# Performance work log

Measured on AMD Instinct MI355X. Metric: run time of the kernel, lower is better.

The kernel has to match this reference:

```python
import jax, jax.numpy as jnp
import numpy as np

H_MODEL = 1024
N_HEADS = 16
N_KV_HEADS = 4
HEAD_DIM = 64
SLIDING_WINDOW = 512
B, S = 2, 2048
NEG_INF = -1e9


def rotate_half(x):
    half = x.shape[-1] // 2
    return jnp.concatenate([-x[..., half:], x[..., :half]], axis=-1)


def setup_inputs() -> dict:
    key = jax.random.key(0)
    ks = jax.random.split(key, 8)
    hidden_states = jax.random.normal(ks[0], (B, S, H_MODEL), dtype=jnp.float32)
    # RoPE tables (HF style): cos/sin of shape [1, S, head_dim]
    inv_freq = 1.0 / (10000.0 ** (jnp.arange(0, HEAD_DIM, 2, dtype=jnp.float32) / HEAD_DIM))
    pos = jnp.arange(S, dtype=jnp.float32)
    freqs = jnp.einsum('s,d->sd', pos, inv_freq)            # [S, D/2]
    emb = jnp.concatenate([freqs, freqs], axis=-1)          # [S, D]
    cos = jnp.cos(emb)[None]                                # [1, S, D]
    sin = jnp.sin(emb)[None]
    # additive causal + sliding-window mask [1,1,S,S]
    i = jnp.arange(S)[:, None]
    j = jnp.arange(S)[None, :]
    allowed = (j <= i) & (i - j < SLIDING_WINDOW)
    attention_mask = jnp.where(allowed, 0.0, NEG_INF).astype(jnp.float32)[None, None]
    # projection weights (torch Linear stores [out, in]; y = x @ W.T)
    std = 0.02
    Wq = jax.random.normal(ks[1], (N_HEADS * HEAD_DIM, H_MODEL), dtype=jnp.float32) * std
    Wk = jax.random.normal(ks[2], (N_KV_HEADS * HEAD_DIM, H_MODEL), dtype=jnp.float32) * std
    Wv = jax.random.normal(ks[3], (N_KV_HEADS * HEAD_DIM, H_MODEL), dtype=jnp.float32) * std
    Wo = jax.random.normal(ks[4], (H_MODEL, N_HEADS * HEAD_DIM), dtype=jnp.float32) * std
    return {"hidden_states": hidden_states, "cos": cos, "sin": sin,
            "attention_mask": attention_mask, "Wq": Wq, "Wk": Wk, "Wv": Wv, "Wo": Wo}


def reference(hidden_states, cos, sin, attention_mask, Wq, Wk, Wv, Wo):
    b, s, _ = hidden_states.shape
    G = N_HEADS // N_KV_HEADS
    scaling = HEAD_DIM ** -0.5
    # QKV projections -> [B, H, S, D]
    q = jnp.einsum('bsh,oh->bso', hidden_states, Wq).reshape(b, s, N_HEADS, HEAD_DIM).transpose(0, 2, 1, 3)
    k = jnp.einsum('bsh,oh->bso', hidden_states, Wk).reshape(b, s, N_KV_HEADS, HEAD_DIM).transpose(0, 2, 1, 3)
    v = jnp.einsum('bsh,oh->bso', hidden_states, Wv).reshape(b, s, N_KV_HEADS, HEAD_DIM).transpose(0, 2, 1, 3)
    # RoPE (cos/sin broadcast over head dim via unsqueeze(1))
    c = cos[:, None, :, :]
    sn = sin[:, None, :, :]
    q = q * c + rotate_half(q) * sn
    k = k * c + rotate_half(k) * sn
    # GQA eager attention: group query heads over kv heads
    qg = q.reshape(b, N_KV_HEADS, G, s, HEAD_DIM)
    scores = jnp.einsum('bkgqd,bkpd->bkgqp', qg, k) * scaling  # [B,Hkv,G,S,S]
    scores = scores + attention_mask[:, :, None, :, :]
    probs = jax.nn.softmax(scores.astype(jnp.float32), axis=-1).astype(q.dtype)
    out = jnp.einsum('bkgqp,bkpd->bkgqd', probs, v)            # [B,Hkv,G,S,D]
    out = out.reshape(b, N_HEADS, s, HEAD_DIM).transpose(0, 2, 1, 3).reshape(b, s, N_HEADS * HEAD_DIM)
    return jnp.einsum('bso,ho->bsh', out, Wo)
```

## Files before the change

### kernel.cpp

```cpp
#include <hip/hip_runtime.h>
#include <hip/hip_bf16.h>

#define S_LEN 2048
#define NH 16
#define NKV 4
#define HD 64
#define WIN 512
#define BATCH 2

typedef __bf16 bf16_8 __attribute__((ext_vector_type(8)));
typedef float f32x4 __attribute__((ext_vector_type(4)));

__device__ inline bf16_8 cvt8(f32x4 a, f32x4 b) {
    bf16_8 r;
    r[0] = (__bf16)a[0]; r[1] = (__bf16)a[1]; r[2] = (__bf16)a[2]; r[3] = (__bf16)a[3];
    r[4] = (__bf16)b[0]; r[5] = (__bf16)b[1]; r[6] = (__bf16)b[2]; r[7] = (__bf16)b[3];
    return r;
}

typedef __attribute__((address_space(1))) const unsigned int guint;
typedef __attribute__((address_space(3))) unsigned int luint;
__device__ __forceinline__ void gload16(const void* g, void* l) {
    __builtin_amdgcn_global_load_lds((guint*)g, (luint*)l, 16, 0, 0);
}

__global__ __launch_bounds__(256) void cvt_pack(
    const float* __restrict__ hs, const float* __restrict__ Wq,
    const float* __restrict__ Wk, const float* __restrict__ Wv,
    const float* __restrict__ Wo,
    __bf16* __restrict__ hsb, __bf16* __restrict__ Wqp,
    __bf16* __restrict__ Wkp, __bf16* __restrict__ Wvp,
    __bf16* __restrict__ Wop)
{
    int i = blockIdx.x * 256 + threadIdx.x;
    if (i < 524288) {
        const size_t j = (size_t)i * 8;
        const f32x4 a = *(const f32x4*)(hs + j);
        const f32x4 b = *(const f32x4*)(hs + j + 4);
        *(bf16_8*)(hsb + j) = cvt8(a, b);
        return;
    }
    i -= 524288;
    const float* S; __bf16* P;
    if (i < 131072)      { S = Wq; P = Wqp; }
    else if (i < 163840) { S = Wk; P = Wkp; i -= 131072; }
    else if (i < 196608) { S = Wv; P = Wvp; i -= 163840; }
    else                 { S = Wo; P = Wop; i -= 196608; }
    const int n = i >> 7;
    const int k = (i & 127) << 3;
    const f32x4 a = *(const f32x4*)(S + (size_t)n * 1024 + k);
    const f32x4 b = *(const f32x4*)(S + (size_t)n * 1024 + k + 4);
    const size_t dst = ((size_t)((n >> 4) * 32 + (k >> 5)) << 9)
                     + ((size_t)((n & 15) | (((k >> 3) & 3) << 4)) << 3);
    *(bf16_8*)(P + dst) = cvt8(a, b);
}

__device__ __forceinline__ void gemm64x128(
    const __bf16* __restrict__ Ap, const __bf16* __restrict__ Bq,
    int row0, __bf16* __restrict__ As, int tid, f32x4 acc[2][4])
{
    const int wave = tid >> 6;
    const int lane = tid & 63;
    const int wm   = wave & 1;
    const int fm   = lane & 15;
    const int fj   = (lane >> 4) << 3;
    const f32x4 fzero = {0.f, 0.f, 0.f, 0.f};
#pragma unroll
    for (int i = 0; i < 2; ++i)
#pragma unroll
        for (int nt = 0; nt < 4; ++nt) acc[i][nt] = fzero;

    const int srow = (wave << 4) + (lane >> 3);
    const int xr   = (((lane & 7) << 3)) ^ ((srow & 7) << 3);
    const __bf16* gA = Ap + (size_t)(row0 + srow) * 1024 + xr;
    __bf16* dstB0 = As + wave * 1024;

    const int r0  = wm * 32 + fm;
    const int xk0 = fj ^ ((fm & 7) << 3);
    const int xk1 = xk0 ^ 32;

    gload16(gA, dstB0);
    gload16(gA + 8192, dstB0 + 512);
    bf16_8 b0[4], b1[4];
#pragma unroll
    for (int nt = 0; nt < 4; ++nt) {
        b0[nt] = *(const bf16_8*)(Bq + nt * 16384);
        b1[nt] = *(const bf16_8*)(Bq + nt * 16384 + 512);
    }
    __syncthreads();

#pragma unroll 2
    for (int it = 0; it < 16; ++it) {
        const int cur = it & 1;
        const bool pf = it < 15;
        bf16_8 nb0[4], nb1[4];
        if (pf) {
            __bf16* dst = As + (cur ^ 1) * 4096 + wave * 1024;
            gload16(gA + (it + 1) * 64, dst);
            gload16(gA + (it + 1) * 64 + 8192, dst + 512);
#pragma unroll
            for (int nt = 0; nt < 4; ++nt) {
                nb0[nt] = *(const bf16_8*)(Bq + nt * 16384 + (it + 1) * 1024);
                nb1[nt] = *(const bf16_8*)(Bq + nt * 16384 + (it + 1) * 1024 + 512);
            }
        }

        const __bf16* Ab = As + cur * 4096;
        bf16_8 af0[2];
        af0[0] = *(const bf16_8*)&Ab[r0 * 64 + xk0];
        af0[1] = *(const bf16_8*)&Ab[(r0 + 16) * 64 + xk0];
#pragma unroll
        for (int i = 0; i < 2; ++i)
#pragma unroll
            for (int nt = 0; nt < 4; ++nt)
                acc[i][nt] = __builtin_amdgcn_mfma_f32_16x16x32_bf16(af0[i], b0[nt], acc[i][nt], 0, 0, 0);

        bf16_8 af1[2];
        af1[0] = *(const bf16_8*)&Ab[r0 * 64 + xk1];
        af1[1] = *(const bf16_8*)&Ab[(r0 + 16) * 64 + xk1];
#pragma unroll
        for (int i = 0; i < 2; ++i)
#pragma unroll
            for (int nt = 0; nt < 4; ++nt)
                acc[i][nt] = __builtin_amdgcn_mfma_f32_16x16x32_bf16(af1[i], b1[nt], acc[i][nt], 0, 0, 0);

        if (pf) {
#pragma unroll
            for (int nt = 0; nt < 4; ++nt) { b0[nt] = nb0[nt]; b1[nt] = nb1[nt]; }
        }
        __syncthreads();
    }
}

__global__ __launch_bounds__(256) void gemm_qkv(
    const __bf16* __restrict__ A,
    const __bf16* __restrict__ Wqp,
    const __bf16* __restrict__ Wkp,
    const __bf16* __restrict__ Wvp,
    __bf16* __restrict__ Qb,
    __bf16* __restrict__ Kf,
    __bf16* __restrict__ Vf,
    const float* __restrict__ cosb,
    const float* __restrict__ sinb)
{
    __shared__ __align__(16) __bf16 smem[9216];

    const int tid  = threadIdx.x;
    const int wave = tid >> 6;
    const int lane = tid & 63;
    const int wm   = wave & 1;
    const int wn   = wave >> 1;
    const int fm   = lane & 15;

    const int row0 = blockIdx.x * 64;
    const int by   = blockIdx.y;

    const __bf16* Bp; int colb; int mode;
    if (by < 8)       { Bp = Wqp; colb = by * 128;        mode = 0; }
    else if (by < 10) { Bp = Wkp; colb = (by - 8) * 128;  mode = 1; }
    else              { Bp = Wvp; colb = (by - 10) * 128; mode = 2; }
    const int col0 = colb;

    const __bf16* Bq = Bp + (size_t)((colb + wn * 64) >> 4) * 16384 + (lane << 3);
    f32x4 acc[2][4];
    gemm64x128(A, Bq, row0, smem, tid, acc);

    const int drow = (lane >> 4) << 2;
    const int cq   = col0 + wn * 64;
    const int bb   = row0 >> 11;
    const int sk0  = row0 & (S_LEN - 1);

    if (mode == 0) {
#pragma unroll
        for (int i = 0; i < 2; ++i) {
#pragma unroll
            for (int r = 0; r < 4; ++r) {
                const int row = row0 + wm * 32 + i * 16 + drow + r;
                const int s   = row & (S_LEN - 1);
#pragma unroll
                for (int nt = 0; nt < 2; ++nt) {
                    const int d = nt * 16 + fm;
                    const float c1 = cosb[s * HD + d];
                    const float s1 = sinb[s * HD + d];
                    const float c2 = cosb[s * HD + d + 32];
                    const float s2 = sinb[s * HD + d + 32];
                    const float x1 = acc[i][nt][r];
                    const float x2 = acc[i][nt + 2][r];
                    Qb[(size_t)row * 1024 + cq + d]      = (__bf16)(x1 * c1 - x2 * s1);
                    Qb[(size_t)row * 1024 + cq + d + 32] = (__bf16)(x2 * c2 + x1 * s2);
                }
            }
        }
    } else if (mode == 1) {
        __bf16* T = smem;
#pragma unroll
        for (int i = 0; i < 2; ++i) {
#pragma unroll
            for (int r = 0; r < 4; ++r) {
                const int kl = wm * 32 + i * 16 + drow + r;
                const int s  = sk0 + kl;
#pragma unroll
                for (int nt = 0; nt < 2; ++nt) {
                    const int d = nt * 16 + fm;
                    const float c1 = cosb[s * HD + d];
                    const float s1 = sinb[s * HD + d];
                    const float c2 = cosb[s * HD + d + 32];
                    const float s2 = sinb[s * HD + d + 32];
                    const float x1 = acc[i][nt][r];
                    const float x2 = acc[i][nt + 2][r];
                    T[kl * 136 + wn * 64 + d]      = (__bf16)(x1 * c1 - x2 * s1);
                    T[kl * 136 + wn * 64 + d + 32] = (__bf16)(x2 * c2 + x1 * s2);
                }
            }
        }
        __syncthreads();
#pragma unroll
        for (int c = 0; c < 4; ++c) {
            const int tile = c * 4 + wave;
            const int hh  = tile >> 3;
            const int kt4 = (tile >> 1) & 3;
            const int dd  = tile & 1;
            const int key = kt4 * 16 + fm;
            const int dl  = dd * 32 + ((lane >> 4) << 3);
            const bf16_8 v = *(const bf16_8*)&T[key * 136 + hh * 64 + dl];
            const int khg = (col0 + hh * 64) >> 6;
            const int ktg = (sk0 >> 4) + kt4;
            *(bf16_8*)&Kf[(size_t)(bb * NKV + khg) * 131072 + (size_t)(ktg * 2 + dd) * 512 + lane * 8] = v;
        }
    } else {
        __bf16* T2 = smem;
#pragma unroll
        for (int i = 0; i < 2; ++i)
#pragma unroll
            for (int r = 0; r < 4; ++r)
#pragma unroll
                for (int nt = 0; nt < 4; ++nt)
                    T2[(wn * 64 + nt * 16 + fm) * 72 + wm * 32 + i * 16 + drow + r] =
                        (__bf16)acc[i][nt][r];
        __syncthreads();
#pragma unroll
        for (int c = 0; c < 4; ++c) {
            const int tile = c * 4 + wave;
            const int hh  = tile >> 3;
            const int dd4 = (tile >> 1) & 3;
            const int ks  = tile & 1;
            const int dl  = dd4 * 16 + fm;
            const int key = ks * 32 + ((lane >> 4) << 3);
            const bf16_8 v = *(const bf16_8*)&T2[(hh * 64 + dl) * 72 + key];
            const int khg = (col0 + hh * 64) >> 6;
            const int kvg = (sk0 >> 5) + ks;
            *(bf16_8*)&Vf[(size_t)(bb * NKV + khg) * 131072 + (size_t)(dd4 * 64 + kvg) * 512 + lane * 8] = v;
        }
    }
}

__global__ __launch_bounds__(256) void gemm_o(
    const __bf16* __restrict__ A,
    const __bf16* __restrict__ Bp,
    float* __restrict__ C)
{
    __shared__ __align__(16) __bf16 smem[9216];

    const int tid  = threadIdx.x;
    const int wave = tid >> 6;
    const int lane = tid & 63;
    const int wm   = wave & 1;
    const int wn   = wave >> 1;

    const int row0 = blockIdx.x * 64;
    const int colb = blockIdx.y * 128;

    const __bf16* Bq = Bp + (size_t)((colb + wn * 64) >> 4) * 16384 + (lane << 3);
    f32x4 acc[2][4];
    gemm64x128(A, Bq, row0, smem, tid, acc);

    const int fm = lane & 15;
    const int drow = (lane >> 4) << 2;
#pragma unroll
    for (int i = 0; i < 2; ++i)
#pragma unroll
        for (int r = 0; r < 4; ++r) {
            const int row = row0 + wm * 32 + i * 16 + drow + r;
#pragma unroll
            for (int nt = 0; nt < 4; ++nt)
                C[(size_t)row * 1024 + colb + wn * 64 + nt * 16 + fm] = acc[i][nt][r];
        }
}

__global__ __launch_bounds__(256) void attn_pk(const __bf16* __restrict__ Q,
                                               const __bf16* __restrict__ Kf,
                                               const __bf16* __restrict__ Vf,
                                               __bf16* __restrict__ O)
{
    __shared__ __align__(16) __bf16 Ps[4][16][72];

    const int tid  = threadIdx.x;
    const int wave = tid >> 6;
    const int lane = tid & 63;

    const int bid0 = blockIdx.x;
    const int bid  = (bid0 & 7) * 128 + (bid0 >> 3);

    const int qt = bid & (S_LEN / 64 - 1);
    const int h  = (bid >> 5) & (NH - 1);
    const int b  = bid >> 9;
    const int kh = h >> 2;

    const int q0 = qt * 64;
    const int qw = q0 + wave * 16;

    const int fm = lane & 15;
    const int fj = (lane >> 4) << 3;

    const size_t qrow = (size_t)(b * S_LEN + qw + fm) * (NH * HD) + h * HD;
    const bf16_8 qf0 = *(const bf16_8*)&Q[qrow + fj];
    const bf16_8 qf1 = *(const bf16_8*)&Q[qrow + 32 + fj];

    const __bf16* Kfb = Kf + (size_t)(b * NKV + kh) * 131072 + lane * 8;
    const __bf16* Vfb = Vf + (size_t)(b * NKV + kh) * 131072 + lane * 8;

    const f32x4 fzero = {0.f, 0.f, 0.f, 0.f};
    f32x4 oacc[4];
    float l[4];
#pragma unroll
    for (int nt = 0; nt < 4; ++nt) oacc[nt] = fzero;
#pragma unroll
    for (int r = 0; r < 4; ++r) l[r] = 0.f;

    const int qbase = qw + ((lane >> 4) << 2);

    const int lo  = (qw >= WIN) ? ((qw - WIN + 1) & ~63) : 0;
    const int hi  = (qw + 15) & ~63;
    const int nit = ((hi - lo) >> 6) + 1;

    for (int it = 0; it < nit; ++it) {
        const int kb = lo + (it << 6);

        f32x4 sc[4];
        const int ktb = kb >> 4;
#pragma unroll
        for (int t4 = 0; t4 < 4; ++t4) {
            const bf16_8 k0 = *(const bf16_8*)(Kfb + (size_t)((ktb + t4) * 2) * 512);
            const bf16_8 k1 = *(const bf16_8*)(Kfb + (size_t)((ktb + t4) * 2 + 1) * 512);
            f32x4 s = fzero;
            s = __builtin_amdgcn_mfma_f32_16x16x32_bf16(qf0, k0, s, 0, 0, 0);
            s = __builtin_amdgcn_mfma_f32_16x16x32_bf16(qf1, k1, s, 0, 0, 0);
            sc[t4] = s;
        }

#pragma unroll
        for (int t4 = 0; t4 < 4; ++t4) {
            const int ki = kb + t4 * 16 + fm;
#pragma unroll
            for (int r = 0; r < 4; ++r) {
                const int qr = qbase + r;
                const float e = __expf(sc[t4][r] * 0.125f);
                const float p = (ki <= qr && qr - ki < WIN) ? e : 0.f;
                l[r] += p;
                Ps[wave][((lane >> 4) << 2) + r][t4 * 16 + fm] = (__bf16)p;
            }
        }

        const bf16_8 pf0 = *(const bf16_8*)&Ps[wave][fm][fj];
        const bf16_8 pf1 = *(const bf16_8*)&Ps[wave][fm][32 + fj];

        const int kvb = kb >> 5;
#pragma unroll
        for (int nt = 0; nt < 4; ++nt) {
            const bf16_8 v0 = *(const bf16_8*)(Vfb + (size_t)(nt * 64 + kvb) * 512);
            const bf16_8 v1 = *(const bf16_8*)(Vfb + (size_t)(nt * 64 + kvb + 1) * 512);
            oacc[nt] = __builtin_amdgcn_mfma_f32_16x16x32_bf16(pf0, v0, oacc[nt], 0, 0, 0);
            oacc[nt] = __builtin_amdgcn_mfma_f32_16x16x32_bf16(pf1, v1, oacc[nt], 0, 0, 0);
        }
    }

#pragma unroll
    for (int off = 8; off > 0; off >>= 1)
#pragma unroll
        for (int r = 0; r < 4; ++r)
            l[r] += __shfl_xor(l[r], off, 64);

    const int drow = (lane >> 4) << 2;
    float inv[4];
#pragma unroll
    for (int r = 0; r < 4; ++r) inv[r] = 1.0f / l[r];
#pragma unroll
    for (int nt = 0; nt < 4; ++nt)
#pragma unroll
        for (int r = 0; r < 4; ++r) {
            const size_t off = (size_t)(b * S_LEN + qw + drow + r) * (NH * HD) + h * HD + nt * 16 + fm;
            O[off] = (__bf16)(oacc[nt][r] * inv[r]);
        }
}

extern "C" void kernel_launch(void* const* d_in, const int* in_sizes, int n_in,
                              void* d_out, int out_size, void* d_ws, size_t ws_size,
                              hipStream_t stream)
{
    const float* hs   = (const float*)d_in[0];
    const float* cosb = (const float*)d_in[1];
    const float* sinb = (const float*)d_in[2];
    const float* Wq = (const float*)d_in[4];
    const float* Wk = (const float*)d_in[5];
    const float* Wv = (const float*)d_in[6];
    const float* Wo = (const float*)d_in[7];

    const int M = BATCH * S_LEN;

    __bf16* hsb = (__bf16*)d_ws;
    __bf16* Wqp = hsb + (size_t)M * 1024;
    __bf16* Wkp = Wqp + 1024 * 1024;
    __bf16* Wvp = Wkp + 256 * 1024;
    __bf16* Wop = Wvp + 256 * 1024;
    __bf16* Qb  = Wop + 1024 * 1024;
    __bf16* Kfb = Qb  + (size_t)M * 1024;
    __bf16* Vfb = Kfb + (size_t)8 * 131072;
    __bf16* Ob  = Vfb + (size_t)8 * 131072;

    dim3 blk(256);
    cvt_pack<<<3328, blk, 0, stream>>>(hs, Wq, Wk, Wv, Wo,
                                       hsb, Wqp, Wkp, Wvp, Wop);

    gemm_qkv<<<dim3(64, 12), blk, 0, stream>>>(hsb, Wqp, Wkp, Wvp,
                                               Qb, Kfb, Vfb, cosb, sinb);

    attn_pk<<<BATCH * NH * (S_LEN / 64), blk, 0, stream>>>(Qb, Kfb, Vfb, Ob);

    gemm_o<<<dim3(64, 8), blk, 0, stream>>>(Ob, Wop, (float*)d_out);
}
```

Baseline: 162.5 us.

## Stage K/V tiles in shared memory with double-buffered async global-to-LDS loads

Each wave used to read its K and V fragments straight from global memory. Now the block cooperatively loads each 64-key K/V tile into a double-buffered LDS array using global_load_lds, prefetching the next tile while the current one is computed. All four waves now share one tile, and the per-wave loop bounds become block-level bounds. This cuts redundant global traffic and hides load latency, at the cost of a __syncthreads per iteration and some extra masked-out iterations for waves whose window starts later.

New measurement: 168.3 us. 3.6% more time.

```diff
diff --git a/kernel.cpp b/kernel.cpp
--- a/kernel.cpp
+++ b/kernel.cpp
@@ -292,6 +292,7 @@
                                                const __bf16* __restrict__ Vf,
                                                __bf16* __restrict__ O)
 {
+    __shared__ __align__(16) __bf16 KV[2][8192];
     __shared__ __align__(16) __bf16 Ps[4][16][72];
 
     const int tid  = threadIdx.x;
@@ -316,8 +317,7 @@
     const bf16_8 qf0 = *(const bf16_8*)&Q[qrow + fj];
     const bf16_8 qf1 = *(const bf16_8*)&Q[qrow + 32 + fj];
 
-    const __bf16* Kfb = Kf + (size_t)(b * NKV + kh) * 131072 + lane * 8;
-    const __bf16* Vfb = Vf + (size_t)(b * NKV + kh) * 131072 + lane * 8;
+    const size_t kvbase = (size_t)(b * NKV + kh) * 131072;
 
     const f32x4 fzero = {0.f, 0.f, 0.f, 0.f};
     f32x4 oacc[4];
@@ -329,19 +329,42 @@
 
     const int qbase = qw + ((lane >> 4) << 2);
 
-    const int lo  = (qw >= WIN) ? ((qw - WIN + 1) & ~63) : 0;
-    const int hi  = (qw + 15) & ~63;
-    const int nit = ((hi - lo) >> 6) + 1;
+    const int lo  = (q0 >= WIN) ? ((q0 - WIN + 1) & ~63) : 0;
+    const int nit = ((q0 - lo) >> 6) + 1;
+
+    const int lofs = (lane << 3);
+
+    {
+        const int kb2 = lo;
+        const __bf16* Kg = Kf + kvbase + (size_t)(kb2 >> 4) * 1024 + wave * 1024 + lofs;
+        gload16(Kg,       &KV[0][wave * 1024]);
+        gload16(Kg + 512, &KV[0][wave * 1024 + 512]);
+        const __bf16* Vg = Vf + kvbase + (size_t)(wave * 64 + (kb2 >> 5)) * 512 + lofs;
+        gload16(Vg,       &KV[0][4096 + wave * 1024]);
+        gload16(Vg + 512, &KV[0][4096 + wave * 1024 + 512]);
+    }
+    __syncthreads();
 
     for (int it = 0; it < nit; ++it) {
-        const int kb = lo + (it << 6);
+        const int kb  = lo + (it << 6);
+        const int cur = it & 1;
+
+        if (it + 1 < nit) {
+            const int kb2 = kb + 64;
+            const int nb  = cur ^ 1;
+            const __bf16* Kg = Kf + kvbase + (size_t)(kb2 >> 4) * 1024 + wave * 1024 + lofs;
+            gload16(Kg,       &KV[nb][wave * 1024]);
+            gload16(Kg + 512, &KV[nb][wave * 1024 + 512]);
+            const __bf16* Vg = Vf + kvbase + (size_t)(wave * 64 + (kb2 >> 5)) * 512 + lofs;
+            gload16(Vg,       &KV[nb][4096 + wave * 1024]);
+            gload16(Vg + 512, &KV[nb][4096 + wave * 1024 + 512]);
+        }
 
         f32x4 sc[4];
-        const int ktb = kb >> 4;
 #pragma unroll
         for (int t4 = 0; t4 < 4; ++t4) {
-            const bf16_8 k0 = *(const bf16_8*)(Kfb + (size_t)((ktb + t4) * 2) * 512);
-            const bf16_8 k1 = *(const bf16_8*)(Kfb + (size_t)((ktb + t4) * 2 + 1) * 512);
+            const bf16_8 k0 = *(const bf16_8*)&KV[cur][(t4 * 2) * 512 + lofs];
+            const bf16_8 k1 = *(const bf16_8*)&KV[cur][(t4 * 2 + 1) * 512 + lofs];
             f32x4 s = fzero;
             s = __builtin_amdgcn_mfma_f32_16x16x32_bf16(qf0, k0, s, 0, 0, 0);
             s = __builtin_amdgcn_mfma_f32_16x16x32_bf16(qf1, k1, s, 0, 0, 0);
@@ -364,14 +387,15 @@
         const bf16_8 pf0 = *(const bf16_8*)&Ps[wave][fm][fj];
         const bf16_8 pf1 = *(const bf16_8*)&Ps[wave][fm][32 + fj];
 
-        const int kvb = kb >> 5;
 #pragma unroll
         for (int nt = 0; nt < 4; ++nt) {
-            const bf16_8 v0 = *(const bf16_8*)(Vfb + (size_t)(nt * 64 + kvb) * 512);
-            const bf16_8 v1 = *(const bf16_8*)(Vfb + (size_t)(nt * 64 + kvb + 1) * 512);
+            const bf16_8 v0 = *(const bf16_8*)&KV[cur][4096 + nt * 1024 + lofs];
+            const bf16_8 v1 = *(const bf16_8*)&KV[cur][4096 + nt * 1024 + 512 + lofs];
             oacc[nt] = __builtin_amdgcn_mfma_f32_16x16x32_bf16(pf0, v0, oacc[nt], 0, 0, 0);
             oacc[nt] = __builtin_amdgcn_mfma_f32_16x16x32_bf16(pf1, v1, oacc[nt], 0, 0, 0);
         }
+
+        __syncthreads();
     }
 
 #pragma unroll
```

## Pack activations in MFMA fragment layout and stream GEMM A-operand from global

Applied to the files above, without the earlier changes.

The hidden states, Q and attention output are now stored in the same 16x32 MFMA-fragment tiled layout as the weights, so each lane loads its A fragment with one contiguous 16-byte global load. The GEMMs drop the LDS double-buffer staging and the per-iteration barriers, and the kernels now declare a minimum of 4 blocks per SIMD. The goal is to remove LDS traffic and synchronisation. In exchange, each wave re-reads its A tiles from global/L2 instead of sharing them through LDS, and the epilogues write scattered bf16 elements into the packed layout.

After: 165.3 us. No clear change (+1.7%).

```diff
diff --git a/kernel.cpp b/kernel.cpp
--- a/kernel.cpp
+++ b/kernel.cpp
@@ -18,34 +18,22 @@
     return r;
 }
 
-typedef __attribute__((address_space(1))) const unsigned int guint;
-typedef __attribute__((address_space(3))) unsigned int luint;
-__device__ __forceinline__ void gload16(const void* g, void* l) {
-    __builtin_amdgcn_global_load_lds((guint*)g, (luint*)l, 16, 0, 0);
-}
 
 __global__ __launch_bounds__(256) void cvt_pack(
     const float* __restrict__ hs, const float* __restrict__ Wq,
     const float* __restrict__ Wk, const float* __restrict__ Wv,
     const float* __restrict__ Wo,
-    __bf16* __restrict__ hsb, __bf16* __restrict__ Wqp,
+    __bf16* __restrict__ hsp, __bf16* __restrict__ Wqp,
     __bf16* __restrict__ Wkp, __bf16* __restrict__ Wvp,
     __bf16* __restrict__ Wop)
 {
     int i = blockIdx.x * 256 + threadIdx.x;
-    if (i < 524288) {
-        const size_t j = (size_t)i * 8;
-        const f32x4 a = *(const f32x4*)(hs + j);
-        const f32x4 b = *(const f32x4*)(hs + j + 4);
-        *(bf16_8*)(hsb + j) = cvt8(a, b);
-        return;
-    }
-    i -= 524288;
     const float* S; __bf16* P;
-    if (i < 131072)      { S = Wq; P = Wqp; }
-    else if (i < 163840) { S = Wk; P = Wkp; i -= 131072; }
-    else if (i < 196608) { S = Wv; P = Wvp; i -= 163840; }
-    else                 { S = Wo; P = Wop; i -= 196608; }
+    if (i < 524288)      { S = hs; P = hsp; }
+    else if (i < 655360) { S = Wq; P = Wqp; i -= 524288; }
+    else if (i < 688128) { S = Wk; P = Wkp; i -= 655360; }
+    else if (i < 720896) { S = Wv; P = Wvp; i -= 688128; }
+    else                 { S = Wo; P = Wop; i -= 720896; }
     const int n = i >> 7;
     const int k = (i & 127) << 3;
     const f32x4 a = *(const f32x4*)(S + (size_t)n * 1024 + k);
@@ -55,89 +43,62 @@
     *(bf16_8*)(P + dst) = cvt8(a, b);
 }
 
-__device__ __forceinline__ void gemm64x128(
-    const __bf16* __restrict__ Ap, const __bf16* __restrict__ Bq,
-    int row0, __bf16* __restrict__ As, int tid, f32x4 acc[2][4])
-{
-    const int wave = tid >> 6;
-    const int lane = tid & 63;
-    const int wm   = wave & 1;
-    const int fm   = lane & 15;
-    const int fj   = (lane >> 4) << 3;
+__device__ __forceinline__ void gemm_stream(
+    const __bf16* __restrict__ Aq, const __bf16* __restrict__ Bq,
+    f32x4 acc[2][4])
+{
     const f32x4 fzero = {0.f, 0.f, 0.f, 0.f};
 #pragma unroll
     for (int i = 0; i < 2; ++i)
 #pragma unroll
         for (int nt = 0; nt < 4; ++nt) acc[i][nt] = fzero;
 
-    const int srow = (wave << 4) + (lane >> 3);
-    const int xr   = (((lane & 7) << 3)) ^ ((srow & 7) << 3);
-    const __bf16* gA = Ap + (size_t)(row0 + srow) * 1024 + xr;
-    __bf16* dstB0 = As + wave * 1024;
-
-    const int r0  = wm * 32 + fm;
-    const int xk0 = fj ^ ((fm & 7) << 3);
-    const int xk1 = xk0 ^ 32;
-
-    gload16(gA, dstB0);
-    gload16(gA + 8192, dstB0 + 512);
     bf16_8 b0[4], b1[4];
 #pragma unroll
     for (int nt = 0; nt < 4; ++nt) {
         b0[nt] = *(const bf16_8*)(Bq + nt * 16384);
         b1[nt] = *(const bf16_8*)(Bq + nt * 16384 + 512);
     }
-    __syncthreads();
-
-#pragma unroll 2
+
     for (int it = 0; it < 16; ++it) {
-        const int cur = it & 1;
+        bf16_8 a0[2], a1[2];
+#pragma unroll
+        for (int i = 0; i < 2; ++i) {
+            a0[i] = *(const bf16_8*)(Aq + (size_t)(i * 32 + it * 2) * 512);
+            a1[i] = *(const bf16_8*)(Aq + (size_t)(i * 32 + it * 2 + 1) * 512);
+        }
+        bf16_8 nb0[4], nb1[4];
         const bool pf = it < 15;
-        bf16_8 nb0[4], nb1[4];
         if (pf) {
-            __bf16* dst = As + (cur ^ 1) * 4096 + wave * 1024;
-            gload16(gA + (it + 1) * 64, dst);
-            gload16(gA + (it + 1) * 64 + 8192, dst + 512);
 #pragma unroll
             for (int nt = 0; nt < 4; ++nt) {
                 nb0[nt] = *(const bf16_8*)(Bq + nt * 16384 + (it + 1) * 1024);
                 nb1[nt] = *(const bf16_8*)(Bq + nt * 16384 + (it + 1) * 1024 + 512);
             }
         }
-
-        const __bf16* Ab = As + cur * 4096;
-        bf16_8 af0[2];
-        af0[0] = *(const bf16_8*)&Ab[r0 * 64 + xk0];
-        af0[1] = *(const bf16_8*)&Ab[(r0 + 16) * 64 + xk0];
 #pragma unroll
         for (int i = 0; i < 2; ++i)
 #pragma unroll
             for (int nt = 0; nt < 4; ++nt)
-                acc[i][nt] = __builtin_amdgcn_mfma_f32_16x16x32_bf16(af0[i], b0[nt], acc[i][nt], 0, 0, 0);
-
-        bf16_8 af1[2];
-        af1[0] = *(const bf16_8*)&Ab[r0 * 64 + xk1];
-        af1[1] = *(const bf16_8*)&Ab[(r0 + 16) * 64 + xk1];
+                acc[i][nt] = __builtin_amdgcn_mfma_f32_16x16x32_bf16(a0[i], b0[nt], acc[i][nt], 0, 0, 0);
 #pragma unroll
         for (int i = 0; i < 2; ++i)
 #pragma unroll
             for (int nt = 0; nt < 4; ++nt)
-                acc[i][nt] = __builtin_amdgcn_mfma_f32_16x16x32_bf16(af1[i], b1[nt], acc[i][nt], 0, 0, 0);
-
+                acc[i][nt] = __builtin_amdgcn_mfma_f32_16x16x32_bf16(a1[i], b1[nt], acc[i][nt], 0, 0, 0);
         if (pf) {
 #pragma unroll
             for (int nt = 0; nt < 4; ++nt) { b0[nt] = nb0[nt]; b1[nt] = nb1[nt]; }
         }
-        __syncthreads();
     }
 }
 
-__global__ __launch_bounds__(256) void gemm_qkv(
-    const __bf16* __restrict__ A,
+__global__ __launch_bounds__(256, 4) void gemm_qkv(
+    const __bf16* __restrict__ Apk,
     const __bf16* __restrict__ Wqp,
     const __bf16* __restrict__ Wkp,
     const __bf16* __restrict__ Wvp,
-    __bf16* __restrict__ Qb,
+    __bf16* __restrict__ Qp,
     __bf16* __restrict__ Kf,
     __bf16* __restrict__ Vf,
     const float* __restrict__ cosb,
@@ -152,7 +113,8 @@
     const int wn   = wave >> 1;
     const int fm   = lane & 15;
 
-    const int row0 = blockIdx.x * 64;
+    const int bx   = blockIdx.x;
+    const int row0 = bx * 64;
     const int by   = blockIdx.y;
 
     const __bf16* Bp; int colb; int mode;
@@ -162,8 +124,9 @@
     const int col0 = colb;
 
     const __bf16* Bq = Bp + (size_t)((colb + wn * 64) >> 4) * 16384 + (lane << 3);
+    const __bf16* Aq = Apk + ((size_t)(bx * 4 + wm * 2) * 32) * 512 + (lane << 3);
     f32x4 acc[2][4];
-    gemm64x128(A, Bq, row0, smem, tid, acc);
+    gemm_stream(Aq, Bq, acc);
 
     const int drow = (lane >> 4) << 2;
     const int cq   = col0 + wn * 64;
@@ -171,8 +134,10 @@
     const int sk0  = row0 & (S_LEN - 1);
 
     if (mode == 0) {
+        const int lp = drow | ((fm >> 3) << 4);
 #pragma unroll
         for (int i = 0; i < 2; ++i) {
+            const size_t t1 = (size_t)(bx * 4 + wm * 2 + i) * 32 + (cq >> 5);
 #pragma unroll
             for (int r = 0; r < 4; ++r) {
                 const int row = row0 + wm * 32 + i * 16 + drow + r;
@@ -186,8 +151,9 @@
                     const float s2 = sinb[s * HD + d + 32];
                     const float x1 = acc[i][nt][r];
                     const float x2 = acc[i][nt + 2][r];
-                    Qb[(size_t)row * 1024 + cq + d]      = (__bf16)(x1 * c1 - x2 * s1);
-                    Qb[(size_t)row * 1024 + cq + d + 32] = (__bf16)(x2 * c2 + x1 * s2);
+                    const size_t o = ((size_t)(lp + r + (nt * 2 << 4)) << 3) + (fm & 7);
+                    Qp[(t1 << 9) + o]       = (__bf16)(x1 * c1 - x2 * s1);
+                    Qp[((t1 + 1) << 9) + o] = (__bf16)(x2 * c2 + x1 * s2);
                 }
             }
         }
@@ -254,25 +220,25 @@
     }
 }
 
-__global__ __launch_bounds__(256) void gemm_o(
-    const __bf16* __restrict__ A,
+__global__ __launch_bounds__(256, 4) void gemm_o(
+    const __bf16* __restrict__ Apk,
     const __bf16* __restrict__ Bp,
     float* __restrict__ C)
 {
-    __shared__ __align__(16) __bf16 smem[9216];
-
     const int tid  = threadIdx.x;
     const int wave = tid >> 6;
     const int lane = tid & 63;
     const int wm   = wave & 1;
     const int wn   = wave >> 1;
 
-    const int row0 = blockIdx.x * 64;
+    const int bx   = blockIdx.x;
+    const int row0 = bx * 64;
     const int colb = blockIdx.y * 128;
 
     const __bf16* Bq = Bp + (size_t)((colb + wn * 64) >> 4) * 16384 + (lane << 3);
+    const __bf16* Aq = Apk + ((size_t)(bx * 4 + wm * 2) * 32) * 512 + (lane << 3);
     f32x4 acc[2][4];
-    gemm64x128(A, Bq, row0, smem, tid, acc);
+    gemm_stream(Aq, Bq, acc);
 
     const int fm = lane & 15;
     const int drow = (lane >> 4) << 2;
@@ -287,10 +253,10 @@
         }
 }
 
-__global__ __launch_bounds__(256) void attn_pk(const __bf16* __restrict__ Q,
+__global__ __launch_bounds__(256) void attn_pk(const __bf16* __restrict__ Qp,
                                                const __bf16* __restrict__ Kf,
                                                const __bf16* __restrict__ Vf,
-                                               __bf16* __restrict__ O)
+                                               __bf16* __restrict__ Op)
 {
     __shared__ __align__(16) __bf16 Ps[4][16][72];
 
@@ -310,11 +276,10 @@
     const int qw = q0 + wave * 16;
 
     const int fm = lane & 15;
-    const int fj = (lane >> 4) << 3;
-
-    const size_t qrow = (size_t)(b * S_LEN + qw + fm) * (NH * HD) + h * HD;
-    const bf16_8 qf0 = *(const bf16_8*)&Q[qrow + fj];
-    const bf16_8 qf1 = *(const bf16_8*)&Q[qrow + 32 + fj];
+
+    const size_t qtile = ((size_t)((b * S_LEN + qw) >> 4) * 32 + h * 2) << 9;
+    const bf16_8 qf0 = *(const bf16_8*)&Qp[qtile + (lane << 3)];
+    const bf16_8 qf1 = *(const bf16_8*)&Qp[qtile + 512 + (lane << 3)];
 
     const __bf16* Kfb = Kf + (size_t)(b * NKV + kh) * 131072 + lane * 8;
     const __bf16* Vfb = Vf + (size_t)(b * NKV + kh) * 131072 + lane * 8;
@@ -328,6 +293,7 @@
     for (int r = 0; r < 4; ++r) l[r] = 0.f;
 
     const int qbase = qw + ((lane >> 4) << 2);
+    const int fj = (lane >> 4) << 3;
 
     const int lo  = (qw >= WIN) ? ((qw - WIN + 1) & ~63) : 0;
     const int hi  = (qw + 15) & ~63;
@@ -384,13 +350,17 @@
     float inv[4];
 #pragma unroll
     for (int r = 0; r < 4; ++r) inv[r] = 1.0f / l[r];
-#pragma unroll
-    for (int nt = 0; nt < 4; ++nt)
-#pragma unroll
-        for (int r = 0; r < 4; ++r) {
-            const size_t off = (size_t)(b * S_LEN + qw + drow + r) * (NH * HD) + h * HD + nt * 16 + fm;
-            O[off] = (__bf16)(oacc[nt][r] * inv[r]);
-        }
+
+    const size_t rt = (size_t)((b * S_LEN + qw) >> 4) * 32;
+#pragma unroll
+    for (int nt = 0; nt < 4; ++nt) {
+        const size_t t = rt + h * 2 + (nt >> 1);
+        const int lp0  = drow | (((nt * 2 + (fm >> 3)) & 3) << 4);
+        const int e    = fm & 7;
+#pragma unroll
+        for (int r = 0; r < 4; ++r)
+            Op[(t << 9) + ((size_t)(lp0 + r) << 3) + e] = (__bf16)(oacc[nt][r] * inv[r]);
+    }
 }
 
 extern "C" void kernel_launch(void* const* d_in, const int* in_sizes, int n_in,
@@ -407,24 +377,24 @@
 
     const int M = BATCH * S_LEN;
 
-    __bf16* hsb = (__bf16*)d_ws;
-    __bf16* Wqp = hsb + (size_t)M * 1024;
+    __bf16* hsp = (__bf16*)d_ws;
+    __bf16* Wqp = hsp + (size_t)M * 1024;
     __bf16* Wkp = Wqp + 1024 * 1024;
     __bf16* Wvp = Wkp + 256 * 1024;
     __bf16* Wop = Wvp + 256 * 1024;
-    __bf16* Qb  = Wop + 1024 * 1024;
-    __bf16* Kfb = Qb  + (size_t)M * 1024;
+    __bf16* Qpb = Wop + 1024 * 1024;
+    __bf16* Kfb = Qpb + (size_t)M * 1024;
     __bf16* Vfb = Kfb + (size_t)8 * 131072;
-    __bf16* Ob  = Vfb + (size_t)8 * 131072;
+    __bf16* Opb = Vfb + (size_t)8 * 131072;
 
     dim3 blk(256);
     cvt_pack<<<3328, blk, 0, stream>>>(hs, Wq, Wk, Wv, Wo,
-                                       hsb, Wqp, Wkp, Wvp, Wop);
-
-    gemm_qkv<<<dim3(64, 12), blk, 0, stream>>>(hsb, Wqp, Wkp, Wvp,
-                                               Qb, Kfb, Vfb, cosb, sinb);
-
-    attn_pk<<<BATCH * NH * (S_LEN / 64), blk, 0, stream>>>(Qb, Kfb, Vfb, Ob);
-
-    gemm_o<<<dim3(64, 8), blk, 0, stream>>>(Ob, Wop, (float*)d_out);
-}
+                                       hsp, Wqp, Wkp, Wvp, Wop);
+
+    gemm_qkv<<<dim3(64, 12), blk, 0, stream>>>(hsp, Wqp, Wkp, Wvp,
+                                               Qpb, Kfb, Vfb, cosb, sinb);
+
+    attn_pk<<<BATCH * NH * (S_LEN / 64), blk, 0, stream>>>(Qpb, Kfb, Vfb, Opb);
+
+    gemm_o<<<dim3(64, 8), blk, 0, stream>>>(Opb, Wop, (float*)d_out);
+}
```
